# Kernel tuning notes

Hardware: AMD Instinct MI355X
Metric: run time of the kernel (lower is better)

Reference implementation:

```python
import jax, jax.numpy as jnp
import numpy as np

N_NODES = 100000
N_EDGES = 1200000
N_DIM = 64


def setup_inputs() -> dict:
    key = jax.random.key(0)
    k1, k2, k3 = jax.random.split(key, 3)
    all_emb = jax.random.normal(k1, (N_NODES, N_DIM), dtype=jnp.float32) * 0.1
    edge_vals = jax.random.uniform(k2, (N_EDGES,), dtype=jnp.float32)
    edge_index = jax.random.randint(k3, (2, N_EDGES), 0, N_NODES, dtype=jnp.int64)
    return {"all_emb": all_emb, "edge_vals": edge_vals, "edge_index": edge_index, "n_layers": 3}


def _spmm(edge_vals, edge_index, x):
    # sparse.mm: out[dst] += val * x[src]; edge_index[0]=row(dst), edge_index[1]=col(src)
    dst, src = edge_index[0], edge_index[1]
    msgs = edge_vals[:, None] * x[src]          # [E, D] gather + scale
    return jax.ops.segment_sum(msgs, dst, num_segments=x.shape[0])


def reference(all_emb, edge_vals, edge_index, n_layers):
    # Fused layer-mean accumulation (avoids stacking all intermediates).
    emb = all_emb
    acc = all_emb
    for _ in range(n_layers):
        emb = _spmm(edge_vals, edge_index, emb)
        acc = acc + emb
    return acc / jnp.float32(n_layers + 1)
```

## Files before the change

kernel.cpp:

```cpp
#include <hip/hip_runtime.h>
#include <hip/hip_bf16.h>
#include <hip/hip_fp16.h>

#define D 64
#define P2_GRID 256
#define KITER 19
#define CHUNK (KITER*256)
#define KMAX 512
#define CAP 4096
#define CASTB 392

__device__ __forceinline__ unsigned f32_to_bf16_rne(float f) {
    unsigned u = __float_as_uint(f);
    return (u + 0x7FFFu + ((u >> 16) & 1u)) >> 16;
}
__device__ __forceinline__ float blo(unsigned w) { return __uint_as_float(w << 16); }
__device__ __forceinline__ float bhi(unsigned w) { return __uint_as_float(w & 0xFFFF0000u); }

__global__ __launch_bounds__(256) void p2_bin_cast(const int* __restrict__ ei,
                                                   const float* __restrict__ vals,
                                                   int* __restrict__ gcur,
                                                   unsigned long long* __restrict__ region,
                                                   const float4* __restrict__ emb4,
                                                   uint2* __restrict__ x0,
                                                   int n4, int E, int K) {
    __shared__ unsigned long long stage[CHUNK];
    __shared__ int hist[KMAX], scanA[KMAX], scanB[KMAX];
    __shared__ int sstart[KMAX], scur[KMAX], sbase[KMAX];

    if (blockIdx.x >= P2_GRID) {
        int i0 = (blockIdx.x - P2_GRID) * 256 + threadIdx.x;
        for (int i = i0; i < n4; i += CASTB * 256) {
            float4 v = emb4[i];
            uint2 o;
            o.x = f32_to_bf16_rne(v.x) | (f32_to_bf16_rne(v.y) << 16);
            o.y = f32_to_bf16_rne(v.z) | (f32_to_bf16_rne(v.w) << 16);
            x0[i] = o;
        }
        return;
    }

    int t  = threadIdx.x;
    int c0 = blockIdx.x * CHUNK;
    int cnt = E - c0; if (cnt > CHUNK) cnt = CHUNK; if (cnt < 0) cnt = 0;

    for (int i = t; i < KMAX; i += 256) hist[i] = 0;
    __syncthreads();

    unsigned long long ent[KITER];
    int eb[KITER];
    #pragma unroll
    for (int k = 0; k < KITER; ++k) {
        int i = t + k * 256;
        eb[k] = -1;
        if (i < cnt) {
            int e   = c0 + i;
            int dst = ei[e];
            int src = ei[E + e];
            unsigned h16 = (unsigned)__half_as_ushort(__float2half(vals[e]));
            int b = dst >> 8;
            eb[k]  = b;
            ent[k] = ((unsigned long long)b << 41)
                   | ((unsigned long long)h16 << 25)
                   | ((unsigned long long)(dst & 0xFF) << 17)
                   | (unsigned long long)src;
            atomicAdd(&hist[b], 1);
        }
    }
    __syncthreads();

    scanA[t] = hist[t]; scanA[t + 256] = hist[t + 256];
    __syncthreads();
    int* pin = scanA; int* pout = scanB;
    for (int off = 1; off < KMAX; off <<= 1) {
        pout[t]       = pin[t]       + (t       >= off ? pin[t - off]       : 0);
        pout[t + 256] = pin[t + 256] + (t + 256 >= off ? pin[t + 256 - off] : 0);
        __syncthreads();
        int* tmp = pin; pin = pout; pout = tmp;
    }
    sstart[t] = pin[t] - hist[t];  sstart[t + 256] = pin[t + 256] - hist[t + 256];
    scur[t]   = sstart[t];         scur[t + 256]   = sstart[t + 256];
    __syncthreads();

    for (int b = t; b < K; b += 256)
        sbase[b] = hist[b] ? atomicAdd(&gcur[b], hist[b]) : 0;

    #pragma unroll
    for (int k = 0; k < KITER; ++k) {
        if (eb[k] >= 0) {
            int pos = atomicAdd(&scur[eb[k]], 1);
            stage[pos] = ent[k];
        }
    }
    __syncthreads();

    for (int i = t; i < cnt; i += 256) {
        unsigned long long e = stage[i];
        int b = (int)(e >> 41);
        int gidx = sbase[b] + (i - sstart[b]);
        if (gidx < CAP)
            region[((size_t)b << 12) | gidx] = e;
    }
}

__global__ __launch_bounds__(256) void p3_csr(const unsigned long long* __restrict__ region,
                                              const int* __restrict__ gcur,
                                              unsigned* __restrict__ gslots,
                                              unsigned* __restrict__ rowinfo,
                                              int N) {
    __shared__ unsigned outstage[CAP];
    __shared__ int rcnt[256], rstart[256], rcur[256], sA[256], sB[256];
    int b = blockIdx.x, t = threadIdx.x;
    int cnt = gcur[b]; if (cnt > CAP) cnt = CAP;
    const unsigned long long* reg = region + ((size_t)b << 12);

    rcnt[t] = 0;
    __syncthreads();

    unsigned long long ent[16];
    int er[16];
    #pragma unroll
    for (int k = 0; k < 16; ++k) {
        int i = t + k * 256;
        er[k] = -1;
        if (i < cnt) {
            ent[k] = reg[i];
            er[k]  = (int)(ent[k] >> 17) & 0xFF;
            atomicAdd(&rcnt[er[k]], 1);
        }
    }
    __syncthreads();

    sA[t] = rcnt[t];
    __syncthreads();
    int* pin = sA; int* pout = sB;
    for (int off = 1; off < 256; off <<= 1) {
        pout[t] = pin[t] + (t >= off ? pin[t - off] : 0);
        __syncthreads();
        int* tmp = pin; pin = pout; pout = tmp;
    }
    rstart[t] = pin[t] - rcnt[t];
    rcur[t]   = rstart[t];
    __syncthreads();

    #pragma unroll
    for (int k = 0; k < 16; ++k) {
        if (er[k] >= 0) {
            int pos = atomicAdd(&rcur[er[k]], 1);
            outstage[pos] = ((unsigned)((ent[k] >> 25) & 0x7FFF) << 17)
                          | (unsigned)(ent[k] & 0x1FFFF);
        }
    }
    __syncthreads();

    size_t gb = (size_t)b << 12;
    for (int i = t; i < cnt; i += 256)
        gslots[gb + i] = outstage[i];
    int row = (b << 8) | t;
    if (row < N) {
        int deg = rcnt[t]; if (deg > 63) deg = 63;
        rowinfo[row] = ((unsigned)(gb + (size_t)rstart[t]) << 6) | (unsigned)deg;
    }
}

__global__ __launch_bounds__(256) void spmm_rows(const unsigned* __restrict__ x2,
                                                 const unsigned* __restrict__ gslots,
                                                 const unsigned* __restrict__ rowinfo,
                                                 unsigned* __restrict__ next2,
                                                 const float2* __restrict__ base2,
                                                 const unsigned* __restrict__ h1buf,
                                                 float2* __restrict__ out2,
                                                 int mode, int N) {
    int gid = blockIdx.x * blockDim.x + threadIdx.x;
    int row = gid >> 6;
    if (row >= N) return;
    int lane = gid & 63;
    int l = lane & 31;
    int h = lane >> 5;
    unsigned info = rowinfo[row];
    int m = (int)(info & 63u);
    const unsigned* s = gslots + (info >> 6);

    float sx = 0.f, sy = 0.f;
    int j = h;
    for (; j + 6 < m; j += 8) {
        unsigned s0 = s[j], s1 = s[j + 2], s2 = s[j + 4], s3 = s[j + 6];
        unsigned w0 = x2[((size_t)(s0 & 0x1FFFF) << 5) | l];
        unsigned w1 = x2[((size_t)(s1 & 0x1FFFF) << 5) | l];
        unsigned w2 = x2[((size_t)(s2 & 0x1FFFF) << 5) | l];
        unsigned w3 = x2[((size_t)(s3 & 0x1FFFF) << 5) | l];
        float v0 = __half2float(__ushort_as_half((unsigned short)(s0 >> 17)));
        float v1 = __half2float(__ushort_as_half((unsigned short)(s1 >> 17)));
        float v2 = __half2float(__ushort_as_half((unsigned short)(s2 >> 17)));
        float v3 = __half2float(__ushort_as_half((unsigned short)(s3 >> 17)));
        sx += v0 * blo(w0);  sy += v0 * bhi(w0);
        sx += v1 * blo(w1);  sy += v1 * bhi(w1);
        sx += v2 * blo(w2);  sy += v2 * bhi(w2);
        sx += v3 * blo(w3);  sy += v3 * bhi(w3);
    }
    for (; j < m; j += 2) {
        unsigned s0 = s[j];
        unsigned w0 = x2[((size_t)(s0 & 0x1FFFF) << 5) | l];
        float v0 = __half2float(__ushort_as_half((unsigned short)(s0 >> 17)));
        sx += v0 * blo(w0);
        sy += v0 * bhi(w0);
    }
    sx += __shfl_xor(sx, 32, 64);
    sy += __shfl_xor(sy, 32, 64);

    size_t o2 = ((size_t)row << 5) | l;
    if (mode != 2) {
        if (h == 1)
            next2[o2] = f32_to_bf16_rne(sx) | (f32_to_bf16_rne(sy) << 16);
    } else if (h == 0) {
        float2 bb = base2[o2];
        unsigned w1 = h1buf[o2];
        unsigned w2 = x2[o2];
        float r0 = (bb.x + blo(w1) + blo(w2) + sx) * 0.25f;
        float r1 = (bb.y + bhi(w1) + bhi(w2) + sy) * 0.25f;
        out2[o2] = make_float2(r0, r1);
    }
}

extern "C" void kernel_launch(void* const* d_in, const int* in_sizes, int n_in,
                              void* d_out, int out_size, void* d_ws, size_t ws_size,
                              hipStream_t stream) {
    const float* all_emb   = (const float*)d_in[0];
    const float* edge_vals = (const float*)d_in[1];
    const int*   edge_idx  = (const int*)d_in[2];

    const int E = in_sizes[1];
    const int n = out_size;
    const int N = n / D;
    const int K = (N + 255) >> 8;
    float* out = (float*)d_out;

    unsigned long long* region = (unsigned long long*)d_ws;
    unsigned* gslots  = (unsigned*)(region + (size_t)K * CAP);
    unsigned* rowinfo = gslots + (size_t)K * CAP;
    int*      gcur    = (int*)(rowinfo + N);
    unsigned* X0      = (unsigned*)(gcur + ((K + 1) & ~1));
    unsigned* X1      = X0 + n / 2;
    unsigned* X2      = X1 + n / 2;

    const int TB = 256;
    const int grid_spmm = (N * 64 + TB - 1) / TB;

    hipMemsetAsync(gcur, 0, (size_t)K * sizeof(int), stream);
    p2_bin_cast<<<P2_GRID + CASTB, TB, 0, stream>>>(edge_idx, edge_vals, gcur, region,
                                                    (const float4*)all_emb, (uint2*)X0,
                                                    n / 4, E, K);
    p3_csr<<<K, TB, 0, stream>>>(region, gcur, gslots, rowinfo, N);

    spmm_rows<<<grid_spmm, TB, 0, stream>>>(X0, gslots, rowinfo, X1,
                                            nullptr, nullptr, nullptr, 0, N);
    spmm_rows<<<grid_spmm, TB, 0, stream>>>(X1, gslots, rowinfo, X2,
                                            nullptr, nullptr, nullptr, 1, N);
    spmm_rows<<<grid_spmm, TB, 0, stream>>>(X2, gslots, rowinfo, nullptr,
                                            (const float2*)all_emb, X1, (float2*)out, 2, N);
}
```

Baseline: 253.1 us.

## Pad CSR rows to multiples of eight and gather one bf16 per lane

The CSR build now pads each row's slot list to a multiple of 8 with zero entries, and stores an iteration count instead of the degree. The SpMM kernel is rewritten so every lane of a 64-wide wavefront owns one feature and processes 8 edges per iteration without a tail loop or cross-half shuffle. The final layer reads the bf16 copy of the input embedding instead of the fp32 original. Padding adds wasted gathers of row 0 and caps per-row degree at 56. The 2-byte per-lane loads may also be less efficient than the previous 4-byte loads.

```diff
diff --git a/kernel.cpp b/kernel.cpp
--- a/kernel.cpp
+++ b/kernel.cpp
@@ -8,14 +8,19 @@
 #define CHUNK (KITER*256)
 #define KMAX 512
 #define CAP 4096
+#define SCAP 4608
 #define CASTB 392
 
 __device__ __forceinline__ unsigned f32_to_bf16_rne(float f) {
     unsigned u = __float_as_uint(f);
     return (u + 0x7FFFu + ((u >> 16) & 1u)) >> 16;
 }
-__device__ __forceinline__ float blo(unsigned w) { return __uint_as_float(w << 16); }
-__device__ __forceinline__ float bhi(unsigned w) { return __uint_as_float(w & 0xFFFF0000u); }
+__device__ __forceinline__ float bfu(unsigned short w) {
+    return __uint_as_float((unsigned)w << 16);
+}
+__device__ __forceinline__ float hv(unsigned s) {
+    return __half2float(__ushort_as_half((unsigned short)(s >> 17)));
+}
 
 __global__ __launch_bounds__(256) void p2_bin_cast(const int* __restrict__ ei,
                                                    const float* __restrict__ vals,
@@ -108,8 +113,9 @@
                                               unsigned* __restrict__ gslots,
                                               unsigned* __restrict__ rowinfo,
                                               int N) {
-    __shared__ unsigned outstage[CAP];
-    __shared__ int rcnt[256], rstart[256], rcur[256], sA[256], sB[256];
+    __shared__ unsigned outstage[SCAP];
+    __shared__ int rcnt[256], rstart[256], rend[256], rcur[256], sA[256], sB[256];
+    __shared__ int stot;
     int b = blockIdx.x, t = threadIdx.x;
     int cnt = gcur[b]; if (cnt > CAP) cnt = CAP;
     const unsigned long long* reg = region + ((size_t)b << 12);
@@ -131,7 +137,9 @@
     }
     __syncthreads();
 
-    sA[t] = rcnt[t];
+    int rc  = rcnt[t]; if (rc > 56) rc = 56;
+    int rcp = (rc + 7) & ~7;
+    sA[t] = rcp;
     __syncthreads();
     int* pin = sA; int* pout = sB;
     for (int off = 1; off < 256; off <<= 1) {
@@ -139,86 +147,80 @@
         __syncthreads();
         int* tmp = pin; pin = pout; pout = tmp;
     }
-    rstart[t] = pin[t] - rcnt[t];
-    rcur[t]   = rstart[t];
+    int rs = pin[t] - rcp;
+    rstart[t] = rs; rcur[t] = rs; rend[t] = rs + rcp;
+    if (t == 255) stot = pin[255];
     __syncthreads();
 
     #pragma unroll
     for (int k = 0; k < 16; ++k) {
         if (er[k] >= 0) {
             int pos = atomicAdd(&rcur[er[k]], 1);
-            outstage[pos] = ((unsigned)((ent[k] >> 25) & 0x7FFF) << 17)
-                          | (unsigned)(ent[k] & 0x1FFFF);
-        }
-    }
-    __syncthreads();
-
-    size_t gb = (size_t)b << 12;
-    for (int i = t; i < cnt; i += 256)
+            if (pos < rend[er[k]] && pos < SCAP)
+                outstage[pos] = ((unsigned)((ent[k] >> 25) & 0x7FFF) << 17)
+                              | (unsigned)(ent[k] & 0x1FFFF);
+        }
+    }
+    for (int i = rs + rc; i < rs + rcp; ++i)
+        if (i >= 0 && i < SCAP) outstage[i] = 0u;
+    __syncthreads();
+
+    int ptot = stot; if (ptot > SCAP) ptot = SCAP;
+    size_t gb = (size_t)b * SCAP;
+    for (int i = t; i < ptot; i += 256)
         gslots[gb + i] = outstage[i];
     int row = (b << 8) | t;
     if (row < N) {
-        int deg = rcnt[t]; if (deg > 63) deg = 63;
-        rowinfo[row] = ((unsigned)(gb + (size_t)rstart[t]) << 6) | (unsigned)deg;
-    }
-}
-
-__global__ __launch_bounds__(256) void spmm_rows(const unsigned* __restrict__ x2,
-                                                 const unsigned* __restrict__ gslots,
-                                                 const unsigned* __restrict__ rowinfo,
-                                                 unsigned* __restrict__ next2,
-                                                 const float2* __restrict__ base2,
-                                                 const unsigned* __restrict__ h1buf,
-                                                 float2* __restrict__ out2,
-                                                 int mode, int N) {
+        int ni = rcp >> 3;
+        if (rs >= SCAP) ni = 0;
+        else if (rs + (ni << 3) > SCAP) ni = (SCAP - rs) >> 3;
+        rowinfo[row] = ((unsigned)(gb + (size_t)rs) << 4) | (unsigned)ni;
+    }
+}
+
+__global__ __launch_bounds__(256) void spmm8(const unsigned short* __restrict__ xs,
+                                             const unsigned* __restrict__ gslots,
+                                             const unsigned* __restrict__ rowinfo,
+                                             unsigned short* __restrict__ nexts,
+                                             const unsigned short* __restrict__ x0s,
+                                             const unsigned short* __restrict__ h1s,
+                                             float* __restrict__ outf,
+                                             int mode, int N) {
     int gid = blockIdx.x * blockDim.x + threadIdx.x;
     int row = gid >> 6;
     if (row >= N) return;
     int lane = gid & 63;
-    int l = lane & 31;
-    int h = lane >> 5;
     unsigned info = rowinfo[row];
-    int m = (int)(info & 63u);
-    const unsigned* s = gslots + (info >> 6);
-
-    float sx = 0.f, sy = 0.f;
-    int j = h;
-    for (; j + 6 < m; j += 8) {
-        unsigned s0 = s[j], s1 = s[j + 2], s2 = s[j + 4], s3 = s[j + 6];
-        unsigned w0 = x2[((size_t)(s0 & 0x1FFFF) << 5) | l];
-        unsigned w1 = x2[((size_t)(s1 & 0x1FFFF) << 5) | l];
-        unsigned w2 = x2[((size_t)(s2 & 0x1FFFF) << 5) | l];
-        unsigned w3 = x2[((size_t)(s3 & 0x1FFFF) << 5) | l];
-        float v0 = __half2float(__ushort_as_half((unsigned short)(s0 >> 17)));
-        float v1 = __half2float(__ushort_as_half((unsigned short)(s1 >> 17)));
-        float v2 = __half2float(__ushort_as_half((unsigned short)(s2 >> 17)));
-        float v3 = __half2float(__ushort_as_half((unsigned short)(s3 >> 17)));
-        sx += v0 * blo(w0);  sy += v0 * bhi(w0);
-        sx += v1 * blo(w1);  sy += v1 * bhi(w1);
-        sx += v2 * blo(w2);  sy += v2 * bhi(w2);
-        sx += v3 * blo(w3);  sy += v3 * bhi(w3);
-    }
-    for (; j < m; j += 2) {
-        unsigned s0 = s[j];
-        unsigned w0 = x2[((size_t)(s0 & 0x1FFFF) << 5) | l];
-        float v0 = __half2float(__ushort_as_half((unsigned short)(s0 >> 17)));
-        sx += v0 * blo(w0);
-        sy += v0 * bhi(w0);
-    }
-    sx += __shfl_xor(sx, 32, 64);
-    sy += __shfl_xor(sy, 32, 64);
-
-    size_t o2 = ((size_t)row << 5) | l;
+    int niter = (int)(info & 15u);
+    const unsigned* s = gslots + (info >> 4);
+
+    float sum = 0.f;
+    for (int it = 0; it < niter; ++it, s += 8) {
+        unsigned s0 = s[0], s1 = s[1], s2 = s[2], s3 = s[3],
+                 s4 = s[4], s5 = s[5], s6 = s[6], s7 = s[7];
+        unsigned short w0 = xs[((size_t)(s0 & 0x1FFFFu) << 6) | lane];
+        unsigned short w1 = xs[((size_t)(s1 & 0x1FFFFu) << 6) | lane];
+        unsigned short w2 = xs[((size_t)(s2 & 0x1FFFFu) << 6) | lane];
+        unsigned short w3 = xs[((size_t)(s3 & 0x1FFFFu) << 6) | lane];
+        unsigned short w4 = xs[((size_t)(s4 & 0x1FFFFu) << 6) | lane];
+        unsigned short w5 = xs[((size_t)(s5 & 0x1FFFFu) << 6) | lane];
+        unsigned short w6 = xs[((size_t)(s6 & 0x1FFFFu) << 6) | lane];
+        unsigned short w7 = xs[((size_t)(s7 & 0x1FFFFu) << 6) | lane];
+        sum += hv(s0) * bfu(w0);
+        sum += hv(s1) * bfu(w1);
+        sum += hv(s2) * bfu(w2);
+        sum += hv(s3) * bfu(w3);
+        sum += hv(s4) * bfu(w4);
+        sum += hv(s5) * bfu(w5);
+        sum += hv(s6) * bfu(w6);
+        sum += hv(s7) * bfu(w7);
+    }
+
+    int o = (row << 6) | lane;
     if (mode != 2) {
-        if (h == 1)
-            next2[o2] = f32_to_bf16_rne(sx) | (f32_to_bf16_rne(sy) << 16);
-    } else if (h == 0) {
-        float2 bb = base2[o2];
-        unsigned w1 = h1buf[o2];
-        unsigned w2 = x2[o2];
-        float r0 = (bb.x + blo(w1) + blo(w2) + sx) * 0.25f;
-        float r1 = (bb.y + bhi(w1) + bhi(w2) + sy) * 0.25f;
-        out2[o2] = make_float2(r0, r1);
+        nexts[o] = (unsigned short)f32_to_bf16_rne(sum);
+    } else {
+        outf[o] = (bfu(x0s[o]) + bfu(h1s[o]) + bfu(xs[o]) + sum) * 0.25f;
     }
 }
 
@@ -237,7 +239,7 @@
 
     unsigned long long* region = (unsigned long long*)d_ws;
     unsigned* gslots  = (unsigned*)(region + (size_t)K * CAP);
-    unsigned* rowinfo = gslots + (size_t)K * CAP;
+    unsigned* rowinfo = gslots + (size_t)K * SCAP;
     int*      gcur    = (int*)(rowinfo + N);
     unsigned* X0      = (unsigned*)(gcur + ((K + 1) & ~1));
     unsigned* X1      = X0 + n / 2;
@@ -252,10 +254,11 @@
                                                     n / 4, E, K);
     p3_csr<<<K, TB, 0, stream>>>(region, gcur, gslots, rowinfo, N);
 
-    spmm_rows<<<grid_spmm, TB, 0, stream>>>(X0, gslots, rowinfo, X1,
-                                            nullptr, nullptr, nullptr, 0, N);
-    spmm_rows<<<grid_spmm, TB, 0, stream>>>(X1, gslots, rowinfo, X2,
-                                            nullptr, nullptr, nullptr, 1, N);
-    spmm_rows<<<grid_spmm, TB, 0, stream>>>(X2, gslots, rowinfo, nullptr,
-                                            (const float2*)all_emb, X1, (float2*)out, 2, N);
-}
+    spmm8<<<grid_spmm, TB, 0, stream>>>((const unsigned short*)X0, gslots, rowinfo,
+                                        (unsigned short*)X1, nullptr, nullptr, nullptr, 0, N);
+    spmm8<<<grid_spmm, TB, 0, stream>>>((const unsigned short*)X1, gslots, rowinfo,
+                                        (unsigned short*)X2, nullptr, nullptr, nullptr, 1, N);
+    spmm8<<<grid_spmm, TB, 0, stream>>>((const unsigned short*)X2, gslots, rowinfo,
+                                        nullptr, (const unsigned short*)X0,
+                                        (const unsigned short*)X1, out, 2, N);
+}
```

Result: faster. 236.9 us (-6.4%).
